# Kernel tuning notes

Hardware: AMD Instinct MI355X
Metric: run time of the kernel (lower is better)

## Reference

```python
import jax, jax.numpy as jnp
import numpy as np

B, T, C, H, K = 2, 4096, 2048, 32, 64
DM, DD, DA = 32, 64, 96
CHUNK = 128
NC = T // CHUNK
GN_EPS = 1e-5 * 8.0 ** 2  # eps * head_size_divisor**2


def setup_inputs() -> dict:
    key = jax.random.key(0)
    ks = iter(jax.random.split(key, 40))
    def nrm(shape, s=1.0):
        return jax.random.normal(next(ks), shape, dtype=jnp.float32) * s
    def uni(shape, lo, hi):
        return jax.random.uniform(next(ks), shape, dtype=jnp.float32, minval=lo, maxval=hi)
    return {
        "x": nrm((B, T, C)),
        "shift_state_in": nrm((B, C)),
        "wkv_state_in": jnp.zeros((B, H, K, K), dtype=jnp.float32),
        "time_maa_x": uni((1, 1, C), 0.0, 1.0),
        "time_maa_w": uni((1, 1, C), 0.0, 1.0),
        "time_maa_k": uni((1, 1, C), 0.0, 1.0),
        "time_maa_v": uni((1, 1, C), 0.0, 1.0),
        "time_maa_r": uni((1, 1, C), 0.0, 1.0),
        "time_maa_g": uni((1, 1, C), 0.0, 1.0),
        "time_maa_a": uni((1, 1, C), 0.0, 1.0),
        "time_maa_w1": nrm((C, 6 * DM), 0.01),
        "time_maa_w2": uni((6, DM, C), -0.01, 0.01),
        "time_decay": uni((1, 1, C), -6.0, -1.0),
        "time_decay_w1": nrm((C, DD), 0.02),
        "time_decay_w2": uni((DD, C), -0.01, 0.01),
        "time_faaaa": nrm((H, K), 0.1),
        "a0": nrm((1, 1, C), 0.01),
        "a1": nrm((C, DA), 0.02),
        "a2": nrm((DA, C), 0.1 / np.sqrt(DA)),
        "k_k": jnp.full((1, 1, C), 0.85, dtype=jnp.float32),
        "k_a": jnp.ones((1, 1, C), dtype=jnp.float32),
        "W_r": nrm((C, C), 1.0 / np.sqrt(C)),
        "W_k": nrm((C, C), 1.0 / np.sqrt(C)),
        "W_v": nrm((C, C), 1.0 / np.sqrt(C)),
        "W_g": nrm((C, C), 1.0 / np.sqrt(C)),
        "W_o": nrm((C, C), 1.0 / np.sqrt(C)),
        "gn_weight": jnp.ones((C,), dtype=jnp.float32),
        "gn_bias": jnp.zeros((C,), dtype=jnp.float32),
    }


def _wkv_delta(r, k, v, w_neg, u, kk, iclr, state0):
    # r,k,v,w_neg,kk,iclr: [B,T,C]; u: [H,K]; state0: [B,H,K,K]
    def to_chunks(t):  # [B,T,C] -> [NC,B,H,CHUNK,K]
        return t.reshape(B, NC, CHUNK, H, K).transpose(1, 0, 3, 2, 4)
    chunks = tuple(map(to_chunks, (r, k, v, w_neg, kk, iclr)))
    u4 = u.reshape(1, H, 1, K)
    mid = CHUNK // 2
    tri = jnp.tril(jnp.ones((CHUNK, CHUNK), dtype=bool), -1)
    eye = jnp.eye(CHUNK, dtype=jnp.float32)

    def step(state, chunk):
        r_c, k_c, v_c, w_log, kk_c, iclr_c = chunk
        w_cum = jnp.cumsum(w_log, axis=2)                       # [B,H,cs,K]
        w_cs = jnp.pad(w_cum[:, :, :-1, :], ((0, 0), (0, 0), (1, 0), (0, 0)))
        offset = w_cs[:, :, mid:mid + 1, :]
        r_decay = jnp.exp(jnp.clip(w_cs - offset, -30, 30))
        k_inv = jnp.exp(jnp.clip(offset - w_cum, -30, 30))
        A = jnp.einsum('bhtk,bhsk->bhts', r_c * r_decay, k_c * k_inv)
        A = jnp.where(tri, A, 0.0)
        diag = jnp.einsum('bhtk,bhtk->bht', r_c, u4 * k_c)
        A = A + diag[..., None] * eye                           # diag_embed add
        kk_corr = jnp.einsum('bhtk,bhsk->bhts', kk_c * iclr_c, kk_c)
        kk_corr = jnp.where(tri, kk_corr, 0.0)
        A_total = A - jnp.tril(A @ kk_corr)
        w_intra = jnp.exp(jnp.clip(w_cum - w_log, -30, 30))
        y = A_total @ v_c + (r_c * w_intra) @ state             # [B,H,cs,K]
        wsum = jnp.sum(w_log, axis=2, keepdims=True)            # [B,H,1,K]
        ws = jnp.exp(wsum)
        w_inter = jnp.exp(jnp.clip(wsum - w_cum, -30, 30))
        kv = jnp.einsum('bhtk,bhtv->bhkv', k_c * w_inter, v_c)
        ab = jnp.einsum('bhtk,bhtj->bhkj', -kk_c * w_inter, kk_c * iclr_c)
        state = state * ws + state @ ab + kv                    # ws broadcasts on dim -2, as in torch
        return state, y

    state, ys = jax.lax.scan(step, state0.astype(jnp.float32), chunks)
    out = ys.transpose(1, 0, 3, 2, 4).reshape(B, T, C)
    return out, state


def reference(x, shift_state_in, wkv_state_in, time_maa_x, time_maa_w, time_maa_k,
              time_maa_v, time_maa_r, time_maa_g, time_maa_a, time_maa_w1, time_maa_w2,
              time_decay, time_decay_w1, time_decay_w2, time_faaaa, a0, a1, a2,
              k_k, k_a, W_r, W_k, W_v, W_g, W_o, gn_weight, gn_bias):
    dxprev = jnp.concatenate([shift_state_in[:, None, :], x[:, :-1]], axis=1) - x
    xxx = jnp.tanh((x + dxprev * time_maa_x) @ time_maa_w1)     # [B,T,6*DM]
    m = jnp.einsum('btsd,sdc->sbtc', xxx.reshape(B, T, 6, DM), time_maa_w2)
    mw, mk, mv, mr, mg, ma = m
    xw = x + dxprev * (time_maa_w + mw)
    xk = x + dxprev * (time_maa_k + mk)
    xv = x + dxprev * (time_maa_v + mv)
    xr = x + dxprev * (time_maa_r + mr)
    xg = x + dxprev * (time_maa_g + mg)
    xa = x + dxprev * (time_maa_a + ma)
    r = xr @ W_r
    k = xk @ W_k
    v = xv @ W_v
    g = jax.nn.silu(xg @ W_g)
    w = time_decay + jnp.tanh(xw @ time_decay_w1) @ time_decay_w2
    iclr = jax.nn.sigmoid(a0 + (xa @ a1) @ a2)
    kk4 = (k * k_k).reshape(B, T, H, K)
    kk = (kk4 / jnp.maximum(jnp.linalg.norm(kk4, axis=-1, keepdims=True), 1e-12)).reshape(B, T, C)
    k = k * (1.0 + (iclr - 1.0) * k_a)
    y, wkv_state_out = _wkv_delta(r, k, v, -jnp.exp(w), time_faaaa, kk, iclr, wkv_state_in)
    # GroupNorm(H groups) over flattened tokens
    yg = y.reshape(B * T, H, K)
    mean = yg.mean(axis=-1, keepdims=True)
    var = yg.var(axis=-1, keepdims=True)
    yg = (yg - mean) / jnp.sqrt(var + GN_EPS)
    y = (yg.reshape(B * T, C) * gn_weight + gn_bias).reshape(B, T, C)
    out = (y * g) @ W_o
    return out, x[:, -1], wkv_state_out
```

## Files before the change

### kernel.cpp

```cpp
#include <hip/hip_runtime.h>


typedef unsigned short u16;
typedef unsigned int   u32;
typedef __attribute__((ext_vector_type(8))) short s16x8;
typedef __attribute__((ext_vector_type(4))) float f32x4;

#define DEV __device__ __forceinline__

DEV float b2f(u16 v){ return __uint_as_float(((u32)v) << 16); }
DEV u16 f2b(float f){ u32 u = __float_as_uint(f); return (u16)((u + 0x7fffu + ((u >> 16) & 1u)) >> 16); }
DEV float clip30(float x){ return fminf(fmaxf(x, -30.f), 30.f); }
DEV void up8(uint4 v, float* f){
  f[0]=b2f((u16)(v.x&0xffffu)); f[1]=b2f((u16)(v.x>>16));
  f[2]=b2f((u16)(v.y&0xffffu)); f[3]=b2f((u16)(v.y>>16));
  f[4]=b2f((u16)(v.z&0xffffu)); f[5]=b2f((u16)(v.z>>16));
  f[6]=b2f((u16)(v.w&0xffffu)); f[7]=b2f((u16)(v.w>>16));
}
DEV uint4 pk8(const float* f){
  uint4 v;
  v.x = (u32)f2b(f[0]) | ((u32)f2b(f[1])<<16);
  v.y = (u32)f2b(f[2]) | ((u32)f2b(f[3])<<16);
  v.z = (u32)f2b(f[4]) | ((u32)f2b(f[5])<<16);
  v.w = (u32)f2b(f[6]) | ((u32)f2b(f[7])<<16);
  return v;
}
DEV void unp16(uint4 v, u16* o){
  o[0]=(u16)(v.x&0xffffu); o[1]=(u16)(v.x>>16);
  o[2]=(u16)(v.y&0xffffu); o[3]=(u16)(v.y>>16);
  o[4]=(u16)(v.z&0xffffu); o[5]=(u16)(v.z>>16);
  o[6]=(u16)(v.w&0xffffu); o[7]=(u16)(v.w>>16);
}
DEV void gload16(const u16* g, u16* l){
  __builtin_amdgcn_global_load_lds(
      (const __attribute__((address_space(1))) u32*)g,
      (__attribute__((address_space(3))) u32*)l, 16, 0, 0);
}
#define ZF4 ((f32x4){0.f,0.f,0.f,0.f})

__global__ void transpose5_k(const float* __restrict__ w0, const float* __restrict__ w1,
    const float* __restrict__ w2, const float* __restrict__ w3, const float* __restrict__ w4,
    u16* __restrict__ o0, u16* __restrict__ o1, u16* __restrict__ o2,
    u16* __restrict__ o3, u16* __restrict__ o4){
  __shared__ float tile[32][33];
  const float* ins[5] = {w0,w1,w2,w3,w4};
  u16* outs[5] = {o0,o1,o2,o3,o4};
  const float* in = ins[blockIdx.z];
  u16* out = outs[blockIdx.z];
  int c0 = blockIdx.x*32, r0 = blockIdx.y*32;
  int tx = threadIdx.x, ty = threadIdx.y;
  #pragma unroll
  for (int j=0;j<4;j++) tile[ty + j*8][tx] = in[(size_t)(r0 + ty + j*8)*2048 + c0 + tx];
  __syncthreads();
  #pragma unroll
  for (int j=0;j<4;j++) out[(size_t)(c0 + ty + j*8)*2048 + r0 + tx] = f2b(tile[tx][ty + j*8]);
}

__global__ void transpose6_k(
    const float* __restrict__ i0, const float* __restrict__ i1, const float* __restrict__ i2,
    const float* __restrict__ i3, const float* __restrict__ i4, const float* __restrict__ i5,
    u16* __restrict__ o0, u16* __restrict__ o1, u16* __restrict__ o2,
    u16* __restrict__ o3, u16* __restrict__ o4, u16* __restrict__ o5){
  __shared__ float tile[32][33];
  const float* ins[6] = {i0,i1,i2,i3,i4,i5};
  u16* outs[6] = {o0,o1,o2,o3,o4,o5};
  const int Rs[6] = {2048, 192, 2048, 64, 2048, 96};
  const int Cs[6] = {192, 2048, 64, 2048, 96, 2048};
  int z = blockIdx.z;
  int R = Rs[z], C = Cs[z];
  int c0 = blockIdx.x*32, r0 = blockIdx.y*32;
  if (c0 >= C || r0 >= R) return;
  const float* in = ins[z];
  u16* out = outs[z];
  int tx = threadIdx.x, ty = threadIdx.y;
  #pragma unroll
  for (int j=0;j<4;j++) tile[ty + j*8][tx] = in[(size_t)(r0 + ty + j*8)*C + c0 + tx];
  __syncthreads();
  #pragma unroll
  for (int j=0;j<4;j++) out[(size_t)(c0 + ty + j*8)*R + r0 + tx] = f2b(tile[tx][ty + j*8]);
}

__global__ __launch_bounds__(256) void prep_k(const float* __restrict__ x, const float* __restrict__ shift,
    const float* __restrict__ maax, u16* __restrict__ xmx, u16* __restrict__ dxp, float* __restrict__ out_xlast){
  int e8 = (blockIdx.x*256 + threadIdx.x) * 8;
  int row = e8 >> 11, col = e8 & 2047;
  int t = row & 4095, b = row >> 12;
  const float* xp = x + (size_t)row*2048 + col;
  const float* pp = t ? (x + (size_t)(row-1)*2048 + col) : (shift + (size_t)b*2048 + col);
  float xf[8], pf[8], mf[8], of[8], df[8];
  *(float4*)(xf)   = *(const float4*)(xp);
  *(float4*)(xf+4) = *(const float4*)(xp+4);
  *(float4*)(pf)   = *(const float4*)(pp);
  *(float4*)(pf+4) = *(const float4*)(pp+4);
  *(float4*)(mf)   = *(const float4*)(maax + col);
  *(float4*)(mf+4) = *(const float4*)(maax + col + 4);
  #pragma unroll
  for (int j=0;j<8;j++){ df[j] = pf[j]-xf[j]; of[j] = xf[j] + df[j]*mf[j]; }
  *(uint4*)(xmx + (size_t)row*2048 + col) = pk8(of);
  *(uint4*)(dxp + (size_t)row*2048 + col) = pk8(df);
  if (t == 4095){
    *(float4*)(out_xlast + (size_t)b*2048 + col)     = *(const float4*)(xf);
    *(float4*)(out_xlast + (size_t)b*2048 + col + 4) = *(const float4*)(xf+4);
  }
}

enum { EPI_STORE=0, EPI_TANH=1, EPI_SILU=2, EPI_LERP=3, EPI_ICLR=5, EPI_STORE32=6 };

__global__ __launch_bounds__(256) void lerp6_k(
    const u16* __restrict__ xxx, const u16* __restrict__ w2t,
    const float* __restrict__ x, const u16* __restrict__ dxp,
    const float* __restrict__ ma0, const float* __restrict__ ma1, const float* __restrict__ ma2,
    const float* __restrict__ ma3, const float* __restrict__ ma4, const float* __restrict__ ma5,
    u16* __restrict__ o0, u16* __restrict__ o1, u16* __restrict__ o2,
    u16* __restrict__ o3, u16* __restrict__ o4, u16* __restrict__ o5)
{
  __shared__ u16 As[128][40];
  __shared__ u16 Bs[128][40];
  const int tid = threadIdx.x, lane = tid & 63, wid = tid >> 6;
  const int m0 = blockIdx.x*128, n0 = blockIdx.y*128;
  const int wrow = (wid>>1)*64, wcol = (wid&1)*64;
  const int fr = lane&15, kg = lane>>4;
  const int r_c0 = tid>>2, r_seg = tid&3, r_c1 = r_c0+64;
  const float* maap[6] = {ma0,ma1,ma2,ma3,ma4,ma5};
  u16* outs[6] = {o0,o1,o2,o3,o4,o5};

  float xv_[4][4][4], dxv_[4][4][4];
  #pragma unroll
  for (int m=0;m<4;m++)
    #pragma unroll
    for (int n=0;n<4;n++)
      #pragma unroll
      for (int q=0;q<4;q++){
        int row = m0 + wrow + m*16 + kg*4 + q;
        int col = n0 + wcol + n*16 + fr;
        xv_[m][n][q]  = x[(size_t)row*2048 + col];
        dxv_[m][n][q] = b2f(dxp[(size_t)row*2048 + col]);
      }

  #pragma unroll
  for (int s=0;s<6;s++){
    __syncthreads();
    *(uint4*)(&As[r_c0][r_seg*8]) = *(const uint4*)(xxx + (size_t)(m0+r_c0)*192 + s*32 + r_seg*8);
    *(uint4*)(&As[r_c1][r_seg*8]) = *(const uint4*)(xxx + (size_t)(m0+r_c1)*192 + s*32 + r_seg*8);
    *(uint4*)(&Bs[r_c0][r_seg*8]) = *(const uint4*)(w2t + (size_t)(n0+r_c0)*192 + s*32 + r_seg*8);
    *(uint4*)(&Bs[r_c1][r_seg*8]) = *(const uint4*)(w2t + (size_t)(n0+r_c1)*192 + s*32 + r_seg*8);
    __syncthreads();
    s16x8 a[4], bb[4];
    #pragma unroll
    for (int m=0;m<4;m++) a[m] = *(const s16x8*)(&As[wrow + m*16 + fr][kg*8]);
    #pragma unroll
    for (int n=0;n<4;n++) bb[n] = *(const s16x8*)(&Bs[wcol + n*16 + fr][kg*8]);
    f32x4 acc[4][4];
    #pragma unroll
    for (int m=0;m<4;m++)
      #pragma unroll
      for (int n=0;n<4;n++) acc[m][n] = ZF4;
    #pragma unroll
    for (int m=0;m<4;m++)
      #pragma unroll
      for (int n=0;n<4;n++)
        acc[m][n] = __builtin_amdgcn_mfma_f32_16x16x32_bf16(a[m], bb[n], acc[m][n], 0,0,0);
    #pragma unroll
    for (int n=0;n<4;n++){
      int col = n0 + wcol + n*16 + fr;
      float mv = maap[s][col];
      #pragma unroll
      for (int m=0;m<4;m++)
        #pragma unroll
        for (int q=0;q<4;q++){
          int row = m0 + wrow + m*16 + kg*4 + q;
          outs[s][(size_t)row*2048 + col] = f2b(xv_[m][n][q] + dxv_[m][n][q]*(mv + acc[m][n][q]));
        }
    }
  }
}

template<int EPI>
__global__ __launch_bounds__(512, 2) void gemm256_k(
    const u16* __restrict__ A, const u16* __restrict__ Bt,
    u16* __restrict__ Cout, float* __restrict__ Cout32,
    int M, int N, int K)
{
  __shared__ __align__(16) u16 lds[4*16384];
  const int tid = threadIdx.x, lane = tid & 63;
  int bxx = blockIdx.x, byy = blockIdx.y;
  if (gridDim.x == 32 && gridDim.y == 8){
    int bid = byy * 32 + bxx;
    int xcd = bid & 7, idx = bid >> 3;
    bxx = xcd*4 + (idx & 3);
    byy = idx >> 2;
  } else {
    int nwg = gridDim.x * gridDim.y;
    if ((nwg & 7) == 0){
      int bid = byy * gridDim.x + bxx;
      int cpx = nwg >> 3;
      int swz = (bid & 7) * cpx + (bid >> 3);
      bxx = swz % gridDim.x; byy = swz / gridDim.x;
    }
  }
  const int m0 = bxx * 256, n0 = byy * 256;
  const int wid = tid >> 6;
  const int wm = wid >> 2, wn = wid & 3;
  const int fr = lane & 15, kg = lane >> 4;
  const int NT = K >> 5;
  const int chunk0 = __builtin_amdgcn_readfirstlane(wid) * 2;
  const int lr = lane >> 2, lsl = lane & 3;
  const int gswz = (lsl ^ ((lr >> 1) & 3)) << 3;
  const int kswz = (kg ^ ((fr >> 1) & 3)) << 3;

  f32x4 acc[8][4];
  #pragma unroll
  for (int m=0;m<8;m++)
    #pragma unroll
    for (int n=0;n<4;n++) acc[m][n] = ZF4;

  auto STAGE = [&](int t){
    u16* ab = lds + (t & 3) * 16384;
    u16* bb = ab + 8192;
    int gc = (t << 5) + gswz;
    #pragma unroll
    for (int i=0;i<2;i++){
      int c = chunk0 + i;
      int r = c*16 + lr;
      gload16(A  + (size_t)(m0 + r)*K + gc, ab + c*512);
      gload16(Bt + (size_t)(n0 + r)*K + gc, bb + c*512);
    }
  };

  STAGE(0); STAGE(1); STAGE(2);
  for (int t=0; t<NT; ++t){
    if (t+2 < NT)      { asm volatile("s_waitcnt vmcnt(8)" ::: "memory"); }
    else if (t+1 < NT) { asm volatile("s_waitcnt vmcnt(4)" ::: "memory"); }
    else               { asm volatile("s_waitcnt vmcnt(0)" ::: "memory"); }
    __builtin_amdgcn_s_barrier();
    __builtin_amdgcn_sched_barrier(0);
    if (t+3 < NT) STAGE(t+3);
    const u16* ab = lds + (t & 3) * 16384;
    const u16* bb = ab + 8192;
    s16x8 af[8], bf[4];
    #pragma unroll
    for (int m=0;m<8;m++){
      int r = wm*128 + m*16 + fr;
      af[m] = *(const s16x8*)(ab + r*32 + kswz);
    }
    #pragma unroll
    for (int n=0;n<4;n++){
      int r = wn*64 + n*16 + fr;
      bf[n] = *(const s16x8*)(bb + r*32 + kswz);
    }
    __builtin_amdgcn_s_setprio(1);
    #pragma unroll
    for (int m=0;m<8;m++)
      #pragma unroll
      for (int n=0;n<4;n++)
        acc[m][n] = __builtin_amdgcn_mfma_f32_16x16x32_bf16(af[m], bf[n], acc[m][n], 0,0,0);
    __builtin_amdgcn_s_setprio(0);
  }

  #pragma unroll
  for (int n=0;n<4;n++){
    int ccol = n0 + wn*64 + n*16 + fr;
    #pragma unroll
    for (int m=0;m<8;m++){
      #pragma unroll
      for (int q=0;q<4;q++){
        int row = m0 + wm*128 + m*16 + kg*4 + q;
        float v = acc[m][n][q];
        size_t oidx = (size_t)row*N + ccol;
        if constexpr (EPI == EPI_STORE) Cout[oidx] = f2b(v);
        else if constexpr (EPI == EPI_STORE32) Cout32[oidx] = v;
        else if constexpr (EPI == EPI_SILU) Cout[oidx] = f2b(v / (1.f + __expf(-v)));
      }
    }
  }
}

template<int EPI, bool ASYNC, bool SWZ>
__global__ __launch_bounds__(256) void gemm_k(
    const u16* __restrict__ A, int lda,
    const u16* __restrict__ Bt, int ldb,
    u16* __restrict__ Cout, float* __restrict__ Cout32, int ldc,
    int M, int N, int K,
    const float* __restrict__ e_x, const u16* __restrict__ e_dxp, const float* __restrict__ e_vec)
{
  constexpr int LDW = ASYNC ? 32 : 40;
  __shared__ u16 As[128][LDW];
  __shared__ u16 Bs[128][LDW];
  const int tid = threadIdx.x;
  const int lane = tid & 63, wid = tid >> 6;
  int bxx = blockIdx.x, byy = blockIdx.y;
  if constexpr (SWZ){
    int nwg = gridDim.x * gridDim.y;
    if ((nwg & 7) == 0){
      int bid = byy * gridDim.x + bxx;
      int cpx = nwg >> 3;
      int swz = (bid & 7) * cpx + (bid >> 3);
      bxx = swz % gridDim.x; byy = swz / gridDim.x;
    }
  }
  const int m0 = bxx * 128, n0 = byy * 128;
  const int wrow = (wid >> 1) * 64, wcol = (wid & 1) * 64;
  const int fr = lane & 15, kg = lane >> 4;
  const int r_c0 = tid >> 2, r_seg = tid & 3;
  const int r_c1 = r_c0 + 64;

  f32x4 acc[4][4];
  #pragma unroll
  for (int m=0;m<4;m++)
    #pragma unroll
    for (int n=0;n<4;n++) acc[m][n] = ZF4;

  for (int k0 = 0; k0 < K; k0 += 32) {
    __syncthreads();
    if constexpr (ASYNC) {
      const int w4 = __builtin_amdgcn_readfirstlane(wid);
      const int rr = lane >> 2, seg8 = (lane & 3) * 8;
      #pragma unroll
      for (int i=0;i<2;i++){
        int row = w4*32 + i*16 + rr;
        gload16(A  + (size_t)(m0 + row)*lda + k0 + seg8, &As[w4*32 + i*16][0]);
        gload16(Bt + (size_t)(n0 + row)*ldb + k0 + seg8, &Bs[w4*32 + i*16][0]);
      }
    } else {
      uint4 av0 = *(const uint4*)(A + (size_t)(m0 + r_c0)*lda + k0 + r_seg*8);
      uint4 av1 = *(const uint4*)(A + (size_t)(m0 + r_c1)*lda + k0 + r_seg*8);
      *(uint4*)(&As[r_c0][r_seg*8]) = av0;
      *(uint4*)(&As[r_c1][r_seg*8]) = av1;
      uint4 z = make_uint4(0,0,0,0);
      uint4 bv0 = (n0 + r_c0 < N) ? *(const uint4*)(Bt + (size_t)(n0 + r_c0)*ldb + k0 + r_seg*8) : z;
      uint4 bv1 = (n0 + r_c1 < N) ? *(const uint4*)(Bt + (size_t)(n0 + r_c1)*ldb + k0 + r_seg*8) : z;
      *(uint4*)(&Bs[r_c0][r_seg*8]) = bv0;
      *(uint4*)(&Bs[r_c1][r_seg*8]) = bv1;
    }
    __syncthreads();
    s16x8 a[4], bb[4];
    #pragma unroll
    for (int m=0;m<4;m++) a[m] = *(const s16x8*)(&As[wrow + m*16 + fr][kg*8]);
    #pragma unroll
    for (int n=0;n<4;n++) bb[n] = *(const s16x8*)(&Bs[wcol + n*16 + fr][kg*8]);
    #pragma unroll
    for (int m=0;m<4;m++)
      #pragma unroll
      for (int n=0;n<4;n++)
        acc[m][n] = __builtin_amdgcn_mfma_f32_16x16x32_bf16(a[m], bb[n], acc[m][n], 0,0,0);
  }
  #pragma unroll
  for (int n=0;n<4;n++){
    int ccol = n0 + wcol + n*16 + fr;
    if (ccol >= N) continue;
    #pragma unroll
    for (int m=0;m<4;m++){
      #pragma unroll
      for (int q=0;q<4;q++){
        int row = m0 + wrow + m*16 + kg*4 + q;
        float v = acc[m][n][q];
        size_t oidx = (size_t)row*ldc + ccol;
        if constexpr (EPI == EPI_STORE) Cout[oidx] = f2b(v);
        else if constexpr (EPI == EPI_STORE32) Cout32[oidx] = v;
        else if constexpr (EPI == EPI_TANH) Cout[oidx] = f2b(tanhf(v));
        else if constexpr (EPI == EPI_SILU) Cout[oidx] = f2b(v / (1.f + expf(-v)));
        else if constexpr (EPI == EPI_LERP){
          float xv = e_x[(size_t)row*2048 + ccol];
          float dx = b2f(e_dxp[(size_t)row*2048 + ccol]);
          Cout[oidx] = f2b(xv + dx * (e_vec[ccol] + v));
        }
        else if constexpr (EPI == EPI_ICLR) Cout[oidx] = f2b(1.f / (1.f + expf(-(e_vec[ccol] + v))));
      }
    }
  }
}

__global__ __launch_bounds__(256) void thin2_k(
    const u16* __restrict__ A0, const u16* __restrict__ Bt0, u16* __restrict__ C0, int N0,
    const u16* __restrict__ A1, const u16* __restrict__ Bt1, u16* __restrict__ C1, int N1,
    int K)
{
  const u16* A  = blockIdx.z ? A1 : A0;
  const u16* Bt = blockIdx.z ? Bt1 : Bt0;
  u16* Cout     = blockIdx.z ? C1 : C0;
  const int N   = blockIdx.z ? N1 : N0;
  const int ldc = N;
  const bool do_tanh = (blockIdx.z == 0);
  const int m0 = blockIdx.x * 64, n0 = blockIdx.y * 64;
  if (n0 >= N) return;

  __shared__ u16 As[64][72];
  __shared__ u16 Bs[64][72];
  const int tid = threadIdx.x;
  const int lane = tid & 63, wid = tid >> 6;
  const int wrow = (wid >> 1) * 32, wcol = (wid & 1) * 32;
  const int fr = lane & 15, kg = lane >> 4;
  const int r_c = tid >> 2, r_seg = tid & 3;

  f32x4 acc[2][2];
  #pragma unroll
  for (int m=0;m<2;m++)
    #pragma unroll
    for (int n=0;n<2;n++) acc[m][n] = ZF4;

  for (int k0 = 0; k0 < K; k0 += 64) {
    __syncthreads();
    {
      const u16* as = A + (size_t)(m0 + r_c)*K + k0 + r_seg*16;
      *(uint4*)(&As[r_c][r_seg*16])     = *(const uint4*)(as);
      *(uint4*)(&As[r_c][r_seg*16 + 8]) = *(const uint4*)(as + 8);
      uint4 z = make_uint4(0,0,0,0);
      bool ok = (n0 + r_c < N);
      const u16* bs = Bt + (size_t)(n0 + r_c)*K + k0 + r_seg*16;
      *(uint4*)(&Bs[r_c][r_seg*16])     = ok ? *(const uint4*)(bs) : z;
      *(uint4*)(&Bs[r_c][r_seg*16 + 8]) = ok ? *(const uint4*)(bs + 8) : z;
    }
    __syncthreads();
    #pragma unroll
    for (int ks=0; ks<2; ++ks){
      s16x8 a[2], bb[2];
      #pragma unroll
      for (int m=0;m<2;m++) a[m] = *(const s16x8*)(&As[wrow + m*16 + fr][ks*32 + kg*8]);
      #pragma unroll
      for (int n=0;n<2;n++) bb[n] = *(const s16x8*)(&Bs[wcol + n*16 + fr][ks*32 + kg*8]);
      #pragma unroll
      for (int m=0;m<2;m++)
        #pragma unroll
        for (int n=0;n<2;n++)
          acc[m][n] = __builtin_amdgcn_mfma_f32_16x16x32_bf16(a[m], bb[n], acc[m][n], 0,0,0);
    }
  }
  #pragma unroll
  for (int n=0;n<2;n++){
    int ccol = n0 + wcol + n*16 + fr;
    if (ccol >= N) continue;
    #pragma unroll
    for (int m=0;m<2;m++){
      #pragma unroll
      for (int q=0;q<4;q++){
        int row = m0 + wrow + m*16 + kg*4 + q;
        float v = acc[m][n][q];
        Cout[(size_t)row*ldc + ccol] = f2b(do_tanh ? tanhf(v) : v);
      }
    }
  }
}

template<int EPI>
__global__ __launch_bounds__(256) void gemm_thin_k(
    const u16* __restrict__ A, int lda,
    const u16* __restrict__ Bt, int ldb,
    u16* __restrict__ Cout, int ldc, int N, int K)
{
  __shared__ u16 As[64][72];
  __shared__ u16 Bs[64][72];
  const int tid = threadIdx.x;
  const int lane = tid & 63, wid = tid >> 6;
  const int m0 = blockIdx.x * 64, n0 = blockIdx.y * 64;
  const int wrow = (wid >> 1) * 32, wcol = (wid & 1) * 32;
  const int fr = lane & 15, kg = lane >> 4;
  const int r_c = tid >> 2, r_seg = tid & 3;

  f32x4 acc[2][2];
  #pragma unroll
  for (int m=0;m<2;m++)
    #pragma unroll
    for (int n=0;n<2;n++) acc[m][n] = ZF4;

  for (int k0 = 0; k0 < K; k0 += 64) {
    __syncthreads();
    {
      const u16* as = A + (size_t)(m0 + r_c)*lda + k0 + r_seg*16;
      *(uint4*)(&As[r_c][r_seg*16])     = *(const uint4*)(as);
      *(uint4*)(&As[r_c][r_seg*16 + 8]) = *(const uint4*)(as + 8);
      uint4 z = make_uint4(0,0,0,0);
      bool ok = (n0 + r_c < N);
      const u16* bs = Bt + (size_t)(n0 + r_c)*ldb + k0 + r_seg*16;
      *(uint4*)(&Bs[r_c][r_seg*16])     = ok ? *(const uint4*)(bs) : z;
      *(uint4*)(&Bs[r_c][r_seg*16 + 8]) = ok ? *(const uint4*)(bs + 8) : z;
    }
    __syncthreads();
    #pragma unroll
    for (int ks=0; ks<2; ++ks){
      s16x8 a[2], bb[2];
      #pragma unroll
      for (int m=0;m<2;m++) a[m] = *(const s16x8*)(&As[wrow + m*16 + fr][ks*32 + kg*8]);
      #pragma unroll
      for (int n=0;n<2;n++) bb[n] = *(const s16x8*)(&Bs[wcol + n*16 + fr][ks*32 + kg*8]);
      #pragma unroll
      for (int m=0;m<2;m++)
        #pragma unroll
        for (int n=0;n<2;n++)
          acc[m][n] = __builtin_amdgcn_mfma_f32_16x16x32_bf16(a[m], bb[n], acc[m][n], 0,0,0);
    }
  }
  #pragma unroll
  for (int n=0;n<2;n++){
    int ccol = n0 + wcol + n*16 + fr;
    if (ccol >= N) continue;
    #pragma unroll
    for (int m=0;m<2;m++){
      #pragma unroll
      for (int q=0;q<4;q++){
        int row = m0 + wrow + m*16 + kg*4 + q;
        float v = acc[m][n][q];
        size_t oidx = (size_t)row*ldc + ccol;
        if constexpr (EPI == EPI_TANH) Cout[oidx] = f2b(tanhf(v));
        else Cout[oidx] = f2b(v);
      }
    }
  }
}

__global__ __launch_bounds__(512, 1) void wkv1_k(
    const u16* __restrict__ r_g, const u16* __restrict__ kraw_g, const u16* __restrict__ v_g,
    const u16* __restrict__ ic_g,
    const u16* __restrict__ t2_g, const u16* __restrict__ dw2t_g, const float* __restrict__ td_g,
    const float* __restrict__ u_g, const float* __restrict__ kkk_g, const float* __restrict__ kka_g,
    u16* __restrict__ y1_g, u16* __restrict__ rw_g,
    u16* __restrict__ kvab_g, float* __restrict__ wsA_g)
{
  __shared__ __align__(16) char arena[162304];
  float* WL   = (float*)(arena);
  float* WC   = (float*)(arena + 34816);
  u16* Abuf   = (u16*)(arena);
  u16* kkcT   = (u16*)(arena + 34816);
  float* diag_l = (float*)(arena + 68096);
  float* offs_l = diag_l + 128;
  float* wsum_l = offs_l + 64;
  float* u_l    = wsum_l + 64;
  float* kkk_l  = u_l + 64;
  float* kka_l  = kkk_l + 64;
  float* td_l   = kka_l + 64;
  u16* rd_l   = (u16*)(arena + 70144);
  u16* vT_l   = (u16*)(arena + 70144);
  u16* ki_l   = (u16*)(arena + 88576);
  u16* kkwT_l = (u16*)(arena + 88576);
  u16* kwT_l  = (u16*)(arena + 107008);
  u16* ka_l   = (u16*)(arena + 125440);
  u16* kkb_l  = (u16*)(arena + 143872);
  u16* kaT_l  = (u16*)(arena + 143872);

  const int tid = threadIdx.x, lane = tid & 63, wid = tid >> 6;
  const int cb = blockIdx.x;
  const int c = cb >> 6, b = (cb >> 5) & 1, h = cb & 31;
  const size_t base = ((size_t)(b*4096 + c*128)) * 2048 + h*64;
  const int fr = lane & 15, kg = lane >> 4;
  const int tq = tid >> 2, kh = (tid & 3) * 16;

  {
    const u16* t2s = t2_g + (size_t)(b*4096 + c*128 + tq)*64 + kh;
    *(uint4*)(&rd_l[tq*72 + kh])     = *(const uint4*)(t2s);
    *(uint4*)(&rd_l[tq*72 + kh + 8]) = *(const uint4*)(t2s + 8);
    int n = tid >> 3, sg2 = (tid & 7) * 8;
    *(uint4*)(&ki_l[n*72 + sg2]) = *(const uint4*)(dw2t_g + (size_t)(h*64 + n)*64 + sg2);
  }
  if (tid < 64){
    u_l[tid]   = u_g[h*64 + tid];
    kkk_l[tid] = kkk_g[h*64 + tid];
    kka_l[tid] = kka_g[h*64 + tid];
    td_l[tid]  = td_g[h*64 + tid];
  }
  __syncthreads();
  {
    f32x4 accW[4];
    #pragma unroll
    for (int n=0;n<4;n++) accW[n] = ZF4;
    #pragma unroll
    for (int ks=0; ks<2; ++ks){
      s16x8 af = *(const s16x8*)(&rd_l[(wid*16 + fr)*72 + ks*32 + kg*8]);
      #pragma unroll
      for (int n=0;n<4;n++){
        s16x8 bf = *(const s16x8*)(&ki_l[(n*16 + fr)*72 + ks*32 + kg*8]);
        accW[n] = __builtin_amdgcn_mfma_f32_16x16x32_bf16(af, bf, accW[n], 0,0,0);
      }
    }
    #pragma unroll
    for (int n=0;n<4;n++)
      #pragma unroll
      for (int q=0;q<4;q++){
        int t = wid*16 + kg*4 + q;
        int s = n*16 + fr;
        WL[t*65 + s] = -__expf(td_l[s] + accW[n][q]);
      }
  }
  __syncthreads();
  for (int j=0;j<8;j++){
    int k = wid*8 + j;
    float v = WL[lane*65 + k];
    #pragma unroll
    for (int d=1; d<64; d<<=1){ float o = __shfl_up(v, d); if (lane >= d) v += o; }
    WC[lane*65 + k] = v;
    float carry = __shfl(v, 63);
    float v2 = WL[(64+lane)*65 + k];
    #pragma unroll
    for (int d=1; d<64; d<<=1){ float o = __shfl_up(v2, d); if (lane >= d) v2 += o; }
    v2 += carry;
    WC[(64+lane)*65 + k] = v2;
    float tot = __shfl(v2, 63);
    if (lane == 0){ offs_l[k] = carry; wsum_l[k] = tot; wsA_g[(size_t)cb*64 + k] = __expf(tot); }
  }
  __syncthreads();
  {
    float rf[16], kf[16], icf[16], kkraw[16];
    const u16* rs  = r_g    + base + (size_t)tq*2048 + kh;
    const u16* ks_ = kraw_g + base + (size_t)tq*2048 + kh;
    const u16* is_ = ic_g   + base + (size_t)tq*2048 + kh;
    up8(*(const uint4*)(rs),     rf);     up8(*(const uint4*)(rs + 8), rf + 8);
    up8(*(const uint4*)(ks_),    kf);     up8(*(const uint4*)(ks_ + 8), kf + 8);
    up8(*(const uint4*)(is_),    icf);    up8(*(const uint4*)(is_ + 8), icf + 8);
    float ss = 0.f;
    #pragma unroll
    for (int e=0;e<16;e++){ kkraw[e] = kf[e]*kkk_l[kh+e]; ss += kkraw[e]*kkraw[e]; }
    ss += __shfl_xor(ss, 1);
    ss += __shfl_xor(ss, 2);
    float rn = 1.f / fmaxf(sqrtf(ss), 1e-12f);
    float dpart = 0.f;
    #pragma unroll
    for (int j=0;j<2;j++){
      float rdf[8], kif[8], rwf[8], kkb8[8], ka8[8];
      #pragma unroll
      for (int e=0;e<8;e++){
        int i = j*8 + e;
        int k = kh + i;
        float kadj = kf[i] * (1.f + (icf[i] - 1.f) * kka_l[k]);
        float wl = WL[tq*65+k], wc = WC[tq*65+k];
        float wcs = wc - wl;
        float off = offs_l[k], wsm = wsum_l[k];
        rdf[e] = rf[i] * __expf(clip30(wcs - off));
        kif[e] = kadj  * __expf(clip30(off - wc));
        rwf[e] = rf[i] * __expf(clip30(wcs));
        kwT_l[k*136 + tq] = f2b(kadj * __expf(clip30(wsm - wc)));
        dpart += rf[i] * u_l[k] * kadj;
        float kkv = kkraw[i]*rn;
        kkb8[e] = kkv; ka8[e] = kkv*icf[i];
      }
      *(uint4*)(&rd_l[tq*72 + kh + j*8])  = pk8(rdf);
      *(uint4*)(&ki_l[tq*72 + kh + j*8])  = pk8(kif);
      *(uint4*)(&kkb_l[tq*72 + kh + j*8]) = pk8(kkb8);
      *(uint4*)(&ka_l [tq*72 + kh + j*8]) = pk8(ka8);
      *(uint4*)(rw_g + base + (size_t)tq*2048 + kh + j*8) = pk8(rwf);
    }
    dpart += __shfl_xor(dpart, 1);
    dpart += __shfl_xor(dpart, 2);
    if ((tid & 3) == 0) diag_l[tq] = dpart;
  }
  __syncthreads();
  f32x4 accA[8];
  #pragma unroll
  for (int n=0;n<8;n++) accA[n] = ZF4;
  #pragma unroll
  for (int ks=0; ks<2; ++ks){
    s16x8 af = *(const s16x8*)(&rd_l[(wid*16 + fr)*72 + ks*32 + kg*8]);
    #pragma unroll
    for (int n=0;n<8;n++){
      s16x8 bf = *(const s16x8*)(&ki_l[(n*16 + fr)*72 + ks*32 + kg*8]);
      accA[n] = __builtin_amdgcn_mfma_f32_16x16x32_bf16(af, bf, accA[n], 0,0,0);
    }
  }
  #pragma unroll
  for (int n=0;n<8;n++)
    #pragma unroll
    for (int q=0;q<4;q++){
      int t = wid*16 + kg*4 + q;
      int s = n*16 + fr;
      float v = accA[n][q];
      v = (t > s) ? v : ((t == s) ? diag_l[t] : 0.f);
      accA[n][q] = v;
      Abuf[t*136 + s] = f2b(v);
    }
  __syncthreads();
  {
    #pragma unroll
    for (int j=0;j<2;j++){
      float kkf[8];
      up8(*(const uint4*)(&kkb_l[tq*72 + kh + j*8]), kkf);
      #pragma unroll
      for (int e=0;e<8;e++){
        int k = kh + j*8 + e;
        kkwT_l[k*136 + tq] = f2b(-kkf[e] * __expf(clip30(wsum_l[k] - WC[tq*65+k])));
      }
    }
  }
  __syncthreads();
  {
    f32x4 accC[8];
    #pragma unroll
    for (int n=0;n<8;n++) accC[n] = ZF4;
    #pragma unroll
    for (int ks=0; ks<2; ++ks){
      s16x8 af = *(const s16x8*)(&ka_l[(wid*16 + fr)*72 + ks*32 + kg*8]);
      #pragma unroll
      for (int n=0;n<8;n++){
        s16x8 bf = *(const s16x8*)(&kkb_l[(n*16 + fr)*72 + ks*32 + kg*8]);
        accC[n] = __builtin_amdgcn_mfma_f32_16x16x32_bf16(af, bf, accC[n], 0,0,0);
      }
    }
    #pragma unroll
    for (int n=0;n<8;n++)
      #pragma unroll
      for (int q=0;q<4;q++){
        int t = wid*16 + kg*4 + q;
        int s = n*16 + fr;
        kkcT[s*136 + t] = f2b((t > s) ? accC[n][q] : 0.f);
      }
  }
  __syncthreads();
  {
    const u16* vs = v_g + base + (size_t)tq*2048 + kh;
    #pragma unroll
    for (int j=0;j<2;j++){
      u16 el[8]; unp16(*(const uint4*)(vs + j*8), el);
      #pragma unroll
      for (int e=0;e<8;e++) vT_l[(kh + j*8 + e)*136 + tq] = el[e];
    }
    #pragma unroll
    for (int j=0;j<2;j++){
      u16 el2[8]; unp16(*(const uint4*)(&ka_l[tq*72 + kh + j*8]), el2);
      #pragma unroll
      for (int e=0;e<8;e++) kaT_l[(kh + j*8 + e)*136 + tq] = el2[e];
    }
  }
  {
    f32x4 accP[8];
    #pragma unroll
    for (int n=0;n<8;n++) accP[n] = ZF4;
    #pragma unroll
    for (int ks=0; ks<4; ++ks){
      s16x8 af = *(const s16x8*)(&Abuf[(wid*16 + fr)*136 + ks*32 + kg*8]);
      #pragma unroll
      for (int n=0;n<8;n++){
        s16x8 bf = *(const s16x8*)(&kkcT[(n*16 + fr)*136 + ks*32 + kg*8]);
        accP[n] = __builtin_amdgcn_mfma_f32_16x16x32_bf16(af, bf, accP[n], 0,0,0);
      }
    }
    #pragma unroll
    for (int n=0;n<8;n++)
      #pragma unroll
      for (int q=0;q<4;q++){
        int t = wid*16 + kg*4 + q;
        int s = n*16 + fr;
        float v = accA[n][q] - ((t >= s) ? accP[n][q] : 0.f);
        Abuf[t*136 + s] = f2b(v);
      }
  }
  __syncthreads();
  {
    f32x4 accY[4];
    #pragma unroll
    for (int n=0;n<4;n++) accY[n] = ZF4;
    #pragma unroll
    for (int ks=0; ks<4; ++ks){
      s16x8 af = *(const s16x8*)(&Abuf[(wid*16 + fr)*136 + ks*32 + kg*8]);
      #pragma unroll
      for (int n=0;n<4;n++){
        s16x8 bf = *(const s16x8*)(&vT_l[(n*16 + fr)*136 + ks*32 + kg*8]);
        accY[n] = __builtin_amdgcn_mfma_f32_16x16x32_bf16(af, bf, accY[n], 0,0,0);
      }
    }
    #pragma unroll
    for (int n=0;n<4;n++)
      #pragma unroll
      for (int q=0;q<4;q++){
        int t = wid*16 + kg*4 + q;
        int vd = n*16 + fr;
        y1_g[base + (size_t)t*2048 + vd] = f2b(accY[n][q]);
      }
  }
  {
    const int isAB = wid >> 2, mrow = (wid & 3) * 16;
    const u16* Amat = isAB ? kkwT_l : kwT_l;
    const u16* Bmat = isAB ? kaT_l  : vT_l;
    f32x4 acc2[4];
    #pragma unroll
    for (int n=0;n<4;n++) acc2[n] = ZF4;
    #pragma unroll
    for (int ks=0; ks<4; ++ks){
      s16x8 af = *(const s16x8*)(&Amat[(mrow + fr)*136 + ks*32 + kg*8]);
      #pragma unroll
      for (int n=0;n<4;n++){
        s16x8 bf = *(const s16x8*)(&Bmat[(n*16 + fr)*136 + ks*32 + kg*8]);
        acc2[n] = __builtin_amdgcn_mfma_f32_16x16x32_bf16(af, bf, acc2[n], 0,0,0);
      }
    }
    u16* kvp = kvab_g + (size_t)cb*8192 + isAB*4096;
    #pragma unroll
    for (int n=0;n<4;n++)
      #pragma unroll
      for (int q=0;q<4;q++){
        int kd = mrow + kg*4 + q, vd = n*16 + fr;
        if (isAB) kvp[vd*64 + kd] = f2b(acc2[n][q]);
        else      kvp[kd*64 + vd] = f2b(acc2[n][q]);
      }
  }
}

__global__ __launch_bounds__(256) void wkv2_k(
   const float* __restrict__ state_in, const u16* __restrict__ kvab_g,
   const float* __restrict__ wsA_g, float* __restrict__ sin_g, float* __restrict__ out_state)
{
  __shared__ u16 Sb[16][72];
  __shared__ u16 abT[64][72];
  const int tid = threadIdx.x, lane = tid & 63, wid = tid >> 6;
  const int blk = blockIdx.x;
  const int bh = blk >> 2, rg = blk & 3;
  const int b = bh >> 5, h = bh & 31;
  const int fr = lane & 15, kg = lane >> 4;
  const int lrow = kg*4;
  const int grow = rg*16 + lrow;
  const int vcol = wid*16 + fr;
  const int vrow = tid >> 2, jc = (tid & 3) * 16;

  f32x4 S;
  #pragma unroll
  for (int q=0;q<4;q++)
    S[q] = state_in[(size_t)bh*4096 + (size_t)(grow+q)*64 + vcol];

  uint4 pf_ab0, pf_ab1; u16 pf_kv[4]; float pf_ws;
  {
    int cb = b*32 + h;
    const u16* kvp = kvab_g + (size_t)cb*8192;
    pf_ab0 = *(const uint4*)(kvp + 4096 + vrow*64 + jc);
    pf_ab1 = *(const uint4*)(kvp + 4096 + vrow*64 + jc + 8);
    #pragma unroll
    for (int q=0;q<4;q++) pf_kv[q] = kvp[(grow+q)*64 + vcol];
    pf_ws = wsA_g[(size_t)cb*64 + vcol];
  }

  for (int c=0;c<32;c++){
    int cb = (c*2+b)*32 + h;
    *(uint4*)(&abT[vrow][jc])   = pf_ab0;
    *(uint4*)(&abT[vrow][jc+8]) = pf_ab1;
    #pragma unroll
    for (int q=0;q<4;q++) Sb[lrow+q][vcol] = f2b(S[q]);
    float kvf[4];
    #pragma unroll
    for (int q=0;q<4;q++) kvf[q] = b2f(pf_kv[q]);
    float wsf = pf_ws;
    float* sip = sin_g + (size_t)cb*4096;
    #pragma unroll
    for (int q=0;q<4;q++) sip[(size_t)(grow+q)*64 + vcol] = S[q];
    __syncthreads();
    if (c < 31){
      int cb2 = ((c+1)*2+b)*32 + h;
      const u16* kvp2 = kvab_g + (size_t)cb2*8192;
      pf_ab0 = *(const uint4*)(kvp2 + 4096 + vrow*64 + jc);
      pf_ab1 = *(const uint4*)(kvp2 + 4096 + vrow*64 + jc + 8);
      #pragma unroll
      for (int q=0;q<4;q++) pf_kv[q] = kvp2[(grow+q)*64 + vcol];
      pf_ws = wsA_g[(size_t)cb2*64 + vcol];
    }
    f32x4 acc = ZF4;
    #pragma unroll
    for (int ks=0; ks<2; ++ks){
      s16x8 a  = *(const s16x8*)(&Sb[fr][ks*32 + kg*8]);
      s16x8 bb = *(const s16x8*)(&abT[wid*16 + fr][ks*32 + kg*8]);
      acc = __builtin_amdgcn_mfma_f32_16x16x32_bf16(a, bb, acc, 0,0,0);
    }
    #pragma unroll
    for (int q=0;q<4;q++)
      S[q] = S[q]*wsf + acc[q] + kvf[q];
    __syncthreads();
  }
  #pragma unroll
  for (int q=0;q<4;q++)
    out_state[(size_t)bh*4096 + (size_t)(grow+q)*64 + vcol] = S[q];
}

__global__ __launch_bounds__(256) void wkv3_k(
   const u16* __restrict__ y1_g, const u16* __restrict__ rw_g,
   const float* __restrict__ sin_g,
   const u16* __restrict__ g_g, const float* __restrict__ gnw, const float* __restrict__ gnb,
   u16* __restrict__ yf_g)
{
  __shared__ float S_l[64][65];
  __shared__ u16 rw_l[128][72];
  int tid = threadIdx.x;
  int cb = blockIdx.x; int c = cb>>6, b = (cb>>5)&1, h = cb&31;
  size_t base = ((size_t)(b*4096 + c*128))*2048 + h*64;
  const float* sip = sin_g + (size_t)cb*4096;
  #pragma unroll
  for (int j=0;j<16;j++){ int flat = tid*16+j; S_l[flat>>6][flat&63] = sip[flat]; }
  {
    int t = tid>>1, kh = (tid&1)*32;
    const u16* rs = rw_g + base + (size_t)t*2048 + kh;
    #pragma unroll
    for (int j=0;j<4;j++) *(uint4*)(&rw_l[t][kh+j*8]) = *(const uint4*)(rs + j*8);
  }
  __syncthreads();
  int t = tid>>1, vh = (tid&1)*32;
  float acc[32];
  #pragma unroll
  for (int j=0;j<32;j++) acc[j] = 0.f;
  for (int kf2=0; kf2<64; kf2++){
    float rv = b2f(rw_l[t][kf2]);
    #pragma unroll
    for (int j=0;j<32;j++) acc[j] += rv * S_l[kf2][vh+j];
  }
  float sum=0.f, sq=0.f;
  float yv[32];
  #pragma unroll
  for (int j=0;j<32;j++){
    yv[j] = acc[j] + b2f(y1_g[base + (size_t)t*2048 + vh + j]);
    sum += yv[j]; sq += yv[j]*yv[j];
  }
  sum += __shfl_xor(sum, 1); sq += __shfl_xor(sq, 1);
  float mean = sum * (1.f/64.f);
  float var = sq * (1.f/64.f) - mean*mean;
  float rstd = rsqrtf(fmaxf(var, 0.f) + 6.4e-4f);
  size_t bt = (size_t)(b*4096 + c*128 + t);
  #pragma unroll
  for (int j=0;j<32;j++){
    int ch = h*64 + vh + j;
    float val = (yv[j]-mean)*rstd * gnw[ch] + gnb[ch];
    val *= b2f(g_g[bt*2048 + ch]);
    yf_g[base + (size_t)t*2048 + vh + j] = f2b(val);
  }
}

#define O_WTR   0ull
#define O_WTK   8388608ull
#define O_WTV   16777216ull
#define O_WTG   25165824ull
#define O_WTO   33554432ull
#define O_W1T   41943040ull
#define O_W2T   42729472ull
#define O_DW1T  43515904ull
#define O_DW2T  43778048ull
#define O_A1T   44040192ull
#define O_A2T   44433408ull
#define O_XXX   44826624ull
#define O_T2    47972352ull
#define O_T3    49020928ull
#define O_WSA   50593792ull
#define O_XMX   51118080ull
#define O_A     84672512ull
#define O_I     118226944ull
#define O_R     151781376ull
#define O_K     185335808ull
#define O_V     218890240ull
#define WS_NEEDED 252444672ull

extern "C" void kernel_launch(void* const* d_in, const int* in_sizes, int n_in,
                              void* d_out, int out_size, void* d_ws, size_t ws_size,
                              hipStream_t stream)
{
  (void)in_sizes; (void)n_in; (void)out_size;
  if (ws_size < WS_NEEDED) return;
  const float* x     = (const float*)d_in[0];
  const float* shift = (const float*)d_in[1];
  const float* st_in = (const float*)d_in[2];
  const float* maax  = (const float*)d_in[3];
  const float* maas[6] = {(const float*)d_in[4],(const float*)d_in[5],(const float*)d_in[6],
                          (const float*)d_in[7],(const float*)d_in[8],(const float*)d_in[9]};
  const float* w1    = (const float*)d_in[10];
  const float* w2    = (const float*)d_in[11];
  const float* td    = (const float*)d_in[12];
  const float* dw1   = (const float*)d_in[13];
  const float* dw2   = (const float*)d_in[14];
  const float* faaaa = (const float*)d_in[15];
  const float* a0v   = (const float*)d_in[16];
  const float* a1w   = (const float*)d_in[17];
  const float* a2w   = (const float*)d_in[18];
  const float* kkk   = (const float*)d_in[19];
  const float* kka   = (const float*)d_in[20];
  const float* Wr    = (const float*)d_in[21];
  const float* Wk    = (const float*)d_in[22];
  const float* Wv    = (const float*)d_in[23];
  const float* Wg    = (const float*)d_in[24];
  const float* Wo    = (const float*)d_in[25];
  const float* gnw   = (const float*)d_in[26];
  const float* gnb   = (const float*)d_in[27];
  float* out = (float*)d_out;
  char* ws = (char*)d_ws;
  #define WSP(o) ((u16*)(ws + (o)))

  u16 *wtR=WSP(O_WTR), *wtK=WSP(O_WTK), *wtV=WSP(O_WTV), *wtG=WSP(O_WTG), *wtO=WSP(O_WTO);
  u16 *w1t=WSP(O_W1T), *w2t=WSP(O_W2T), *dw1t=WSP(O_DW1T), *dw2t=WSP(O_DW2T), *a1t=WSP(O_A1T), *a2t=WSP(O_A2T);
  u16 *xxx=WSP(O_XXX), *t2b=WSP(O_T2), *t3b=WSP(O_T3);
  u16 *sXMX=WSP(O_XMX), *sA=WSP(O_A), *sI=WSP(O_I), *sR=WSP(O_R), *sK=WSP(O_K), *sV=WSP(O_V);
  u16 *rw = WSP(O_WTR);
  float* sinF = (float*)(ws + O_XMX);
  float* wsA = (float*)(ws + O_WSA);
  float* out_xlast = out + 16777216;
  float* out_state = out + 16781312;

  dim3 tb(32,8);
  transpose5_k<<<dim3(64,64,5), tb, 0, stream>>>(Wr, Wk, Wv, Wg, Wo, wtR, wtK, wtV, wtG, wtO);
  transpose6_k<<<dim3(64,64,6), tb, 0, stream>>>(w1, w2, dw1, dw2, a1w, a2w,
                                                 w1t, w2t, dw1t, dw2t, a1t, a2t);

  prep_k<<<8192, 256, 0, stream>>>(x, shift, maax, sXMX , sI , out_xlast);

  gemm_thin_k<EPI_TANH><<<dim3(128,3), 256, 0, stream>>>(sXMX, 2048, w1t, 2048, xxx, 192, 192, 2048);
  lerp6_k<<<dim3(64,16), 256, 0, stream>>>(xxx, w2t, x, sI ,
      maas[0], maas[1], maas[2], maas[3], maas[4], maas[5],
      sXMX , sA , sR , sK , sV , sI );
  thin2_k<<<dim3(128,2,2), 256, 0, stream>>>(sXMX, dw1t, t2b, 64, sI, a1t, t3b, 96, 2048);
  gemm_k<EPI_ICLR,true,true><<<dim3(64,16), 256, 0, stream>>>(t3b, 96, a2t, 96, sI, nullptr, 2048, 8192, 2048, 96, nullptr, nullptr, a0v);
  gemm256_k<EPI_STORE><<<dim3(32,8), 512, 0, stream>>>(sK, wtR, sXMX, nullptr, 8192, 2048, 2048);
  gemm256_k<EPI_STORE><<<dim3(32,8), 512, 0, stream>>>(sA, wtK, sK, nullptr, 8192, 2048, 2048);
  gemm256_k<EPI_STORE><<<dim3(32,8), 512, 0, stream>>>(sR, wtV, sA, nullptr, 8192, 2048, 2048);
  gemm256_k<EPI_SILU><<<dim3(32,8), 512, 0, stream>>>(sV, wtG, sR, nullptr, 8192, 2048, 2048);
  wkv1_k<<<2048, 512, 0, stream>>>(sXMX, sK, sA, sI, t2b, dw2t, td, faaaa, kkk, kka,
                                   sK, rw, sV, wsA);
  wkv2_k<<<256, 256, 0, stream>>>(st_in, sV, wsA, sinF, out_state);
  wkv3_k<<<2048, 256, 0, stream>>>(sK, rw, sinF, sR , gnw, gnb, sK );
  gemm256_k<EPI_STORE32><<<dim3(32,8), 512, 0, stream>>>(sK, wtO, nullptr, out, 8192, 2048, 2048);
}
```

Baseline: 937.2 us.

## Run 256x256 GEMM with 16 waves and route iclr projection through it

```diff
diff --git a/kernel.cpp b/kernel.cpp
--- a/kernel.cpp
+++ b/kernel.cpp
@@ -176,10 +176,10 @@
 }
 
 template<int EPI>
-__global__ __launch_bounds__(512, 2) void gemm256_k(
+__global__ __launch_bounds__(1024) void gemm256_k(
     const u16* __restrict__ A, const u16* __restrict__ Bt,
     u16* __restrict__ Cout, float* __restrict__ Cout32,
-    int M, int N, int K)
+    int M, int N, int K, const float* __restrict__ e_vec)
 {
   __shared__ __align__(16) u16 lds[4*16384];
   const int tid = threadIdx.x, lane = tid & 63;
@@ -203,14 +203,14 @@
   const int wm = wid >> 2, wn = wid & 3;
   const int fr = lane & 15, kg = lane >> 4;
   const int NT = K >> 5;
-  const int chunk0 = __builtin_amdgcn_readfirstlane(wid) * 2;
+  const int wchunk = __builtin_amdgcn_readfirstlane(wid);
   const int lr = lane >> 2, lsl = lane & 3;
   const int gswz = (lsl ^ ((lr >> 1) & 3)) << 3;
   const int kswz = (kg ^ ((fr >> 1) & 3)) << 3;
 
-  f32x4 acc[8][4];
-  #pragma unroll
-  for (int m=0;m<8;m++)
+  f32x4 acc[4][4];
+  #pragma unroll
+  for (int m=0;m<4;m++)
     #pragma unroll
     for (int n=0;n<4;n++) acc[m][n] = ZF4;
 
@@ -218,29 +218,27 @@
     u16* ab = lds + (t & 3) * 16384;
     u16* bb = ab + 8192;
     int gc = (t << 5) + gswz;
-    #pragma unroll
-    for (int i=0;i<2;i++){
-      int c = chunk0 + i;
-      int r = c*16 + lr;
-      gload16(A  + (size_t)(m0 + r)*K + gc, ab + c*512);
-      gload16(Bt + (size_t)(n0 + r)*K + gc, bb + c*512);
-    }
+    int r = wchunk*16 + lr;
+    gload16(A  + (size_t)(m0 + r)*K + gc, ab + wchunk*512);
+    gload16(Bt + (size_t)(n0 + r)*K + gc, bb + wchunk*512);
   };
 
-  STAGE(0); STAGE(1); STAGE(2);
+  STAGE(0);
+  if (NT > 1) STAGE(1);
+  if (NT > 2) STAGE(2);
   for (int t=0; t<NT; ++t){
-    if (t+2 < NT)      { asm volatile("s_waitcnt vmcnt(8)" ::: "memory"); }
-    else if (t+1 < NT) { asm volatile("s_waitcnt vmcnt(4)" ::: "memory"); }
+    if (t+2 < NT)      { asm volatile("s_waitcnt vmcnt(4)" ::: "memory"); }
+    else if (t+1 < NT) { asm volatile("s_waitcnt vmcnt(2)" ::: "memory"); }
     else               { asm volatile("s_waitcnt vmcnt(0)" ::: "memory"); }
     __builtin_amdgcn_s_barrier();
     __builtin_amdgcn_sched_barrier(0);
     if (t+3 < NT) STAGE(t+3);
     const u16* ab = lds + (t & 3) * 16384;
     const u16* bb = ab + 8192;
-    s16x8 af[8], bf[4];
-    #pragma unroll
-    for (int m=0;m<8;m++){
-      int r = wm*128 + m*16 + fr;
+    s16x8 af[4], bf[4];
+    #pragma unroll
+    for (int m=0;m<4;m++){
+      int r = wm*64 + m*16 + fr;
       af[m] = *(const s16x8*)(ab + r*32 + kswz);
     }
     #pragma unroll
@@ -250,7 +248,7 @@
     }
     __builtin_amdgcn_s_setprio(1);
     #pragma unroll
-    for (int m=0;m<8;m++)
+    for (int m=0;m<4;m++)
       #pragma unroll
       for (int n=0;n<4;n++)
         acc[m][n] = __builtin_amdgcn_mfma_f32_16x16x32_bf16(af[m], bf[n], acc[m][n], 0,0,0);
@@ -261,110 +259,16 @@
   for (int n=0;n<4;n++){
     int ccol = n0 + wn*64 + n*16 + fr;
     #pragma unroll
-    for (int m=0;m<8;m++){
+    for (int m=0;m<4;m++){
       #pragma unroll
       for (int q=0;q<4;q++){
-        int row = m0 + wm*128 + m*16 + kg*4 + q;
+        int row = m0 + wm*64 + m*16 + kg*4 + q;
         float v = acc[m][n][q];
         size_t oidx = (size_t)row*N + ccol;
         if constexpr (EPI == EPI_STORE) Cout[oidx] = f2b(v);
         else if constexpr (EPI == EPI_STORE32) Cout32[oidx] = v;
         else if constexpr (EPI == EPI_SILU) Cout[oidx] = f2b(v / (1.f + __expf(-v)));
-      }
-    }
-  }
-}
-
-template<int EPI, bool ASYNC, bool SWZ>
-__global__ __launch_bounds__(256) void gemm_k(
-    const u16* __restrict__ A, int lda,
-    const u16* __restrict__ Bt, int ldb,
-    u16* __restrict__ Cout, float* __restrict__ Cout32, int ldc,
-    int M, int N, int K,
-    const float* __restrict__ e_x, const u16* __restrict__ e_dxp, const float* __restrict__ e_vec)
-{
-  constexpr int LDW = ASYNC ? 32 : 40;
-  __shared__ u16 As[128][LDW];
-  __shared__ u16 Bs[128][LDW];
-  const int tid = threadIdx.x;
-  const int lane = tid & 63, wid = tid >> 6;
-  int bxx = blockIdx.x, byy = blockIdx.y;
-  if constexpr (SWZ){
-    int nwg = gridDim.x * gridDim.y;
-    if ((nwg & 7) == 0){
-      int bid = byy * gridDim.x + bxx;
-      int cpx = nwg >> 3;
-      int swz = (bid & 7) * cpx + (bid >> 3);
-      bxx = swz % gridDim.x; byy = swz / gridDim.x;
-    }
-  }
-  const int m0 = bxx * 128, n0 = byy * 128;
-  const int wrow = (wid >> 1) * 64, wcol = (wid & 1) * 64;
-  const int fr = lane & 15, kg = lane >> 4;
-  const int r_c0 = tid >> 2, r_seg = tid & 3;
-  const int r_c1 = r_c0 + 64;
-
-  f32x4 acc[4][4];
-  #pragma unroll
-  for (int m=0;m<4;m++)
-    #pragma unroll
-    for (int n=0;n<4;n++) acc[m][n] = ZF4;
-
-  for (int k0 = 0; k0 < K; k0 += 32) {
-    __syncthreads();
-    if constexpr (ASYNC) {
-      const int w4 = __builtin_amdgcn_readfirstlane(wid);
-      const int rr = lane >> 2, seg8 = (lane & 3) * 8;
-      #pragma unroll
-      for (int i=0;i<2;i++){
-        int row = w4*32 + i*16 + rr;
-        gload16(A  + (size_t)(m0 + row)*lda + k0 + seg8, &As[w4*32 + i*16][0]);
-        gload16(Bt + (size_t)(n0 + row)*ldb + k0 + seg8, &Bs[w4*32 + i*16][0]);
-      }
-    } else {
-      uint4 av0 = *(const uint4*)(A + (size_t)(m0 + r_c0)*lda + k0 + r_seg*8);
-      uint4 av1 = *(const uint4*)(A + (size_t)(m0 + r_c1)*lda + k0 + r_seg*8);
-      *(uint4*)(&As[r_c0][r_seg*8]) = av0;
-      *(uint4*)(&As[r_c1][r_seg*8]) = av1;
-      uint4 z = make_uint4(0,0,0,0);
-      uint4 bv0 = (n0 + r_c0 < N) ? *(const uint4*)(Bt + (size_t)(n0 + r_c0)*ldb + k0 + r_seg*8) : z;
-      uint4 bv1 = (n0 + r_c1 < N) ? *(const uint4*)(Bt + (size_t)(n0 + r_c1)*ldb + k0 + r_seg*8) : z;
-      *(uint4*)(&Bs[r_c0][r_seg*8]) = bv0;
-      *(uint4*)(&Bs[r_c1][r_seg*8]) = bv1;
-    }
-    __syncthreads();
-    s16x8 a[4], bb[4];
-    #pragma unroll
-    for (int m=0;m<4;m++) a[m] = *(const s16x8*)(&As[wrow + m*16 + fr][kg*8]);
-    #pragma unroll
-    for (int n=0;n<4;n++) bb[n] = *(const s16x8*)(&Bs[wcol + n*16 + fr][kg*8]);
-    #pragma unroll
-    for (int m=0;m<4;m++)
-      #pragma unroll
-      for (int n=0;n<4;n++)
-        acc[m][n] = __builtin_amdgcn_mfma_f32_16x16x32_bf16(a[m], bb[n], acc[m][n], 0,0,0);
-  }
-  #pragma unroll
-  for (int n=0;n<4;n++){
-    int ccol = n0 + wcol + n*16 + fr;
-    if (ccol >= N) continue;
-    #pragma unroll
-    for (int m=0;m<4;m++){
-      #pragma unroll
-      for (int q=0;q<4;q++){
-        int row = m0 + wrow + m*16 + kg*4 + q;
-        float v = acc[m][n][q];
-        size_t oidx = (size_t)row*ldc + ccol;
-        if constexpr (EPI == EPI_STORE) Cout[oidx] = f2b(v);
-        else if constexpr (EPI == EPI_STORE32) Cout32[oidx] = v;
-        else if constexpr (EPI == EPI_TANH) Cout[oidx] = f2b(tanhf(v));
-        else if constexpr (EPI == EPI_SILU) Cout[oidx] = f2b(v / (1.f + expf(-v)));
-        else if constexpr (EPI == EPI_LERP){
-          float xv = e_x[(size_t)row*2048 + ccol];
-          float dx = b2f(e_dxp[(size_t)row*2048 + ccol]);
-          Cout[oidx] = f2b(xv + dx * (e_vec[ccol] + v));
-        }
-        else if constexpr (EPI == EPI_ICLR) Cout[oidx] = f2b(1.f / (1.f + expf(-(e_vec[ccol] + v))));
+        else if constexpr (EPI == EPI_ICLR) Cout[oidx] = f2b(1.f / (1.f + __expf(-(e_vec[ccol] + v))));
       }
     }
   }
@@ -992,14 +896,14 @@
       maas[0], maas[1], maas[2], maas[3], maas[4], maas[5],
       sXMX , sA , sR , sK , sV , sI );
   thin2_k<<<dim3(128,2,2), 256, 0, stream>>>(sXMX, dw1t, t2b, 64, sI, a1t, t3b, 96, 2048);
-  gemm_k<EPI_ICLR,true,true><<<dim3(64,16), 256, 0, stream>>>(t3b, 96, a2t, 96, sI, nullptr, 2048, 8192, 2048, 96, nullptr, nullptr, a0v);
-  gemm256_k<EPI_STORE><<<dim3(32,8), 512, 0, stream>>>(sK, wtR, sXMX, nullptr, 8192, 2048, 2048);
-  gemm256_k<EPI_STORE><<<dim3(32,8), 512, 0, stream>>>(sA, wtK, sK, nullptr, 8192, 2048, 2048);
-  gemm256_k<EPI_STORE><<<dim3(32,8), 512, 0, stream>>>(sR, wtV, sA, nullptr, 8192, 2048, 2048);
-  gemm256_k<EPI_SILU><<<dim3(32,8), 512, 0, stream>>>(sV, wtG, sR, nullptr, 8192, 2048, 2048);
+  gemm256_k<EPI_ICLR><<<dim3(32,8), 1024, 0, stream>>>(t3b, a2t, sI, nullptr, 8192, 2048, 96, a0v);
+  gemm256_k<EPI_STORE><<<dim3(32,8), 1024, 0, stream>>>(sK, wtR, sXMX, nullptr, 8192, 2048, 2048, nullptr);
+  gemm256_k<EPI_STORE><<<dim3(32,8), 1024, 0, stream>>>(sA, wtK, sK, nullptr, 8192, 2048, 2048, nullptr);
+  gemm256_k<EPI_STORE><<<dim3(32,8), 1024, 0, stream>>>(sR, wtV, sA, nullptr, 8192, 2048, 2048, nullptr);
+  gemm256_k<EPI_SILU><<<dim3(32,8), 1024, 0, stream>>>(sV, wtG, sR, nullptr, 8192, 2048, 2048, nullptr);
   wkv1_k<<<2048, 512, 0, stream>>>(sXMX, sK, sA, sI, t2b, dw2t, td, faaaa, kkk, kka,
                                    sK, rw, sV, wsA);
   wkv2_k<<<256, 256, 0, stream>>>(st_in, sV, wsA, sinF, out_state);
   wkv3_k<<<2048, 256, 0, stream>>>(sK, rw, sinF, sR , gnw, gnb, sK );
-  gemm256_k<EPI_STORE32><<<dim3(32,8), 512, 0, stream>>>(sK, wtO, nullptr, out, 8192, 2048, 2048);
-}
+  gemm256_k<EPI_STORE32><<<dim3(32,8), 1024, 0, stream>>>(sK, wtO, nullptr, out, 8192, 2048, 2048, nullptr);
+}
```

New measurement: 902.5 us. -3.7%, faster.
